# Kernel optimization log

Hardware: AMD Instinct MI355X
Metric: run time of the kernel (lower is better)

Reference implementation:

```python
import jax, jax.numpy as jnp
import numpy as np
from jax import lax

EPS = 1e-4
DN = ('NDHWC', 'DHWIO', 'NDHWC')


def _m(mask, dtype):
    return mask[..., None].astype(dtype)


def bn_relu(x, mask):
    # BatchNorm1d over active voxels only (training-mode batch stats, gamma=1, beta=0), then ReLU.
    m = _m(mask, x.dtype)
    n = jnp.sum(m)
    mean = jnp.sum(x * m, axis=(0, 1, 2, 3)) / n
    xc = (x - mean) * m  # re-mask: inactive voxels stay exactly zero
    var = jnp.sum(xc * xc, axis=(0, 1, 2, 3)) / n
    return jnp.maximum(xc * lax.rsqrt(var + EPS), 0.0)


def subm3(x, w, mask):
    # SubMConv3d k=3 pad=1: dense conv on zero-at-inactive input, output restricted to active sites.
    y = lax.conv_general_dilated(x, w, (1, 1, 1), 'SAME', dimension_numbers=DN)
    return y * _m(mask, x.dtype)


def down2(x, w):
    # SparseConv3d k=2 s=2: non-overlapping windows; inactive inputs are zero so dense strided conv matches.
    return lax.conv_general_dilated(x, w, (2, 2, 2), 'VALID', dimension_numbers=DN)


def pool_mask(mask):
    B, D, H, W = mask.shape
    return jnp.any(mask.reshape(B, D // 2, 2, H // 2, 2, W // 2, 2), axis=(2, 4, 6))


def up2(x, w, mask):
    # SparseInverseConv3d k=2 (indice_key inverse of the stride-2 conv): conv-transpose masked to original indices.
    y = jnp.einsum('bdhwc,ijkco->bdihjwko', x, w)
    B, Dc, _, Hc, _, Wc, _, Co = y.shape
    return y.reshape(B, 2 * Dc, 2 * Hc, 2 * Wc, Co) * _m(mask, x.dtype)


def resblock(x, mask, wa, wb, w_sc=None):
    # ResidualBlock: i_branch (identity or 1x1 Custom1x1Subm3d: feats @ W.T) + BN-ReLU-SubM-BN-ReLU-SubM.
    idb = x if w_sc is None else jnp.einsum('bdhwc,oc->bdhwo', x, w_sc)
    h = bn_relu(x, mask)
    h = subm3(h, wa, mask)
    h = bn_relu(h, mask)
    h = subm3(h, wb, mask)
    return h + idb


def unet_forward(x, mask, w_in, w_b1a, w_b1b, w_d1, w_b2a, w_b2b, w_d2,
                 w_b3a, w_b3b, w_u2, w_t2_sc, w_t2a, w_t2b, w_u1, w_t1_sc, w_t1a, w_t1b):
    mask2 = pool_mask(mask)
    mask3 = pool_mask(mask2)
    x0 = subm3(x, w_in, mask)                 # input_conv (subm1)
    x1 = resblock(x0, mask, w_b1a, w_b1b)     # level-1 block (32->32)
    d1 = down2(bn_relu(x1, mask), w_d1)       # BN-ReLU + stride-2 conv 32->64
    x2 = resblock(d1, mask2, w_b2a, w_b2b)    # level-2 block (64->64)
    d2 = down2(bn_relu(x2, mask2), w_d2)      # 64->96
    x3 = resblock(d2, mask3, w_b3a, w_b3b)    # bottom level (96->96)
    u2 = up2(bn_relu(x3, mask3), w_u2, mask2)  # BN-ReLU + inverse conv 96->64
    t2 = resblock(jnp.concatenate([x2, u2], -1), mask2, w_t2a, w_t2b, w_t2_sc)  # tail 128->64
    u1 = up2(bn_relu(t2, mask2), w_u1, mask)   # 64->32
    t1 = resblock(jnp.concatenate([x1, u1], -1), mask, w_t1a, w_t1b, w_t1_sc)   # tail 64->32
    return bn_relu(t1, mask)                   # output_layer: BN + ReLU


def setup_inputs() -> dict:
    key = jax.random.key(0)
    ks = jax.random.split(key, 20)
    B, D = 1, 48
    Cin, C1, C2, C3 = 6, 32, 64, 96
    mask = jax.random.uniform(ks[0], (B, D, D, D)) < 0.12
    x = jax.random.normal(ks[1], (B, D, D, D, Cin), jnp.float32) * mask[..., None]

    def w(k, shape):
        fan = float(np.prod(shape[:-1]))
        return (jax.random.normal(k, shape, jnp.float32) / np.sqrt(fan)).astype(jnp.float32)

    return {
        'x': x, 'mask': mask,
        'w_in': w(ks[2], (3, 3, 3, Cin, C1)),
        'w_b1a': w(ks[3], (3, 3, 3, C1, C1)), 'w_b1b': w(ks[4], (3, 3, 3, C1, C1)),
        'w_d1': w(ks[5], (2, 2, 2, C1, C2)),
        'w_b2a': w(ks[6], (3, 3, 3, C2, C2)), 'w_b2b': w(ks[7], (3, 3, 3, C2, C2)),
        'w_d2': w(ks[8], (2, 2, 2, C2, C3)),
        'w_b3a': w(ks[9], (3, 3, 3, C3, C3)), 'w_b3b': w(ks[10], (3, 3, 3, C3, C3)),
        'w_u2': w(ks[11], (2, 2, 2, C3, C2)),
        'w_t2_sc': w(ks[12], (C2, 2 * C2)),
        'w_t2a': w(ks[13], (3, 3, 3, 2 * C2, C2)), 'w_t2b': w(ks[14], (3, 3, 3, C2, C2)),
        'w_u1': w(ks[15], (2, 2, 2, C2, C1)),
        'w_t1_sc': w(ks[16], (C1, 2 * C1)),
        'w_t1a': w(ks[17], (3, 3, 3, 2 * C1, C1)), 'w_t1b': w(ks[18], (3, 3, 3, C1, C1)),
    }


def reference(x, mask, w_in, w_b1a, w_b1b, w_d1, w_b2a, w_b2b, w_d2,
              w_b3a, w_b3b, w_u2, w_t2_sc, w_t2a, w_t2b, w_u1, w_t1_sc, w_t1a, w_t1b):
    return unet_forward(x, mask, w_in, w_b1a, w_b1b, w_d1, w_b2a, w_b2b, w_d2,
                        w_b3a, w_b3b, w_u2, w_t2_sc, w_t2a, w_t2b, w_u1, w_t1_sc, w_t1a, w_t1b)
```

## Files before the change

kernel.cpp:

```cpp
#include <hip/hip_runtime.h>


typedef short bf16x8 __attribute__((ext_vector_type(8)));
typedef float f32x4 __attribute__((ext_vector_type(4)));
typedef unsigned short ushort_t;

constexpr int D1 = 48, DIM2 = 24, DIM3 = 12;
constexpr int N1 = D1 * D1 * D1;
constexpr int N2 = DIM2 * DIM2 * DIM2;
constexpr int N3 = DIM3 * DIM3 * DIM3;

constexpr size_t OFF_A      = 0;
constexpr size_t OFF_R1     = 3538944;
constexpr size_t OFF_CAT1   = 7077888;
constexpr size_t OFF_D1R    = 14155776;
constexpr size_t OFF_R3     = 15040512;
constexpr size_t OFF_CAT2   = 15925248;
constexpr size_t OFF_D2R    = 17694720;
constexpr size_t OFF_R4     = 17860608;
constexpr size_t OFF_X3R    = 18026496;
constexpr size_t OFF_BN1_32 = 18192384;
constexpr size_t OFF_BN1_64 = 19961920;
constexpr size_t OFF_BN2_64 = 23500928;
constexpr size_t OFF_BN2_128= 23943360;
constexpr size_t OFF_BN3_96 = 24828160;
constexpr size_t OFF_BFEND  = 24911168;
constexpr size_t OFF_WT     = 24911168;
constexpr size_t OFF_STATS  = 25634112;
constexpr size_t STATS_FLOATS = 15 * 2048 * 2;
constexpr size_t OFF_CNT    = OFF_STATS + STATS_FLOATS;
constexpr size_t OFF_L1     = OFF_CNT + 16;
constexpr size_t OFF_L2     = OFF_L1 + N1;
constexpr size_t OFF_L3     = OFF_L2 + N2;
constexpr size_t OFF_M1     = OFF_L3 + N3;
constexpr size_t OFF_M2     = OFF_M1 + N1 / 4;
constexpr size_t OFF_M3     = OFF_M2 + N2 / 4;

constexpr int WTS[16] = {0, 32768, 65536, 98304, 114688, 229376, 344064,
                         393216, 669696, 946176, 1175552, 1290240, 1347584,
                         1380352, 1429504, 1445888};

__device__ inline ushort_t f2bf(float f) {
  union { float f; unsigned u; } x; x.f = f;
  unsigned u = x.u + 0x7FFF + ((x.u >> 16) & 1);
  return (ushort_t)(u >> 16);
}

__global__ __launch_bounds__(256) void k_mask1(const float* __restrict__ x,
                                               unsigned char* __restrict__ m,
                                               int* __restrict__ list, int* __restrict__ cnt) {
  int v = blockIdx.x * 256 + threadIdx.x;
  if (v >= N1) return;
  const float* p = x + (size_t)v * 6;
  bool a = (p[0] != 0.f) || (p[1] != 0.f) || (p[2] != 0.f) ||
           (p[3] != 0.f) || (p[4] != 0.f) || (p[5] != 0.f);
  m[v] = a ? 1 : 0;
  if (a) { int pos = atomicAdd(cnt, 1); list[pos] = v; }
}

__global__ __launch_bounds__(256) void k_pool(const unsigned char* __restrict__ mf,
                                              unsigned char* __restrict__ mc,
                                              int* __restrict__ list, int* __restrict__ cnt, int DC) {
  int v = blockIdx.x * 256 + threadIdx.x;
  int n = DC * DC * DC;
  if (v >= n) return;
  int w = v % DC, h = (v / DC) % DC, d = v / (DC * DC);
  int DF = 2 * DC;
  bool a = false;
  for (int i = 0; i < 2; i++)
    for (int j = 0; j < 2; j++)
      for (int k = 0; k < 2; k++)
        a |= (mf[(size_t)(((2 * d + i) * DF + (2 * h + j)) * DF + (2 * w + k))] != 0);
  mc[v] = a ? 1 : 0;
  if (a) { int pos = atomicAdd(cnt, 1); list[pos] = v; }
}

struct WJobs {
  const float* src[15];
  int start[16];
  short cinr[15], cipad[15], cout[15], kk[15];
};

__global__ __launch_bounds__(256) void k_wprep(WJobs jb, ushort_t* __restrict__ wt, int total) {
  int gid = blockIdx.x * 256 + threadIdx.x;
  if (gid >= total) return;
  int j = 0;
#pragma unroll
  for (int jj = 0; jj < 15; jj++)
    if (gid >= jb.start[jj + 1]) j = jj + 1;
  int e = gid - jb.start[j];
  int CIP = jb.cipad[j], CO = jb.cout[j], CIR = jb.cinr[j], KKr = jb.kk[j];
  int ci = e % CIP;
  int co = (e / CIP) % CO;
  int k = e / (CIP * CO);
  float v = (k < KKr && ci < CIR) ? jb.src[j][((size_t)k * CIR + ci) * CO + co] : 0.f;
  wt[gid] = f2bf(v);
}

__global__ __launch_bounds__(256) void k_xprep(const float* __restrict__ x, ushort_t* __restrict__ xp) {
  int gid = blockIdx.x * 256 + threadIdx.x;
  if (gid >= (N1 + 4) * 8) return;
  int v = gid >> 3, c = (gid & 7) * 4;
  uint2 o = make_uint2(0u, 0u);
  if (v < N1) {
    ushort_t u[4];
#pragma unroll
    for (int j = 0; j < 4; j++) {
      int ci = c + j;
      float f = (ci < 6) ? x[(size_t)v * 6 + ci] : 0.f;
      u[j] = f2bf(f);
    }
    o.x = (unsigned)u[0] | ((unsigned)u[1] << 16);
    o.y = (unsigned)u[2] | ((unsigned)u[3] << 16);
  }
  *(uint2*)&xp[(size_t)v * 32 + c] = o;
}

template <int CIPAD, int COUT, int KK, bool UP>
__global__ __launch_bounds__(512, 2) void k_conv6(
    const ushort_t* __restrict__ in, const ushort_t* __restrict__ wt,
    float* __restrict__ out, int ostride, int ooff,
    const float* __restrict__ res, int rstride,
    double* __restrict__ st,
    const int* __restrict__ list, const int* __restrict__ cnt, int DD) {
  constexpr int KCH = CIPAD / 32;
  constexpr int TPS = (KK + 3) / 4;
  __shared__ float red[8][8][64];
  __shared__ float fin[32][33];
  __shared__ int vidx[32];

  int n = cnt[0];
  int base = blockIdx.x * 32;
  if (base >= n) return;
  int t = threadIdx.x, wv = t >> 6, ln = t & 63;
  int vg = wv & 1, ks = wv >> 1;
  int fr = ln & 15, kg = ln >> 4;
  int coblk = blockIdx.y * 32;
  if (t < 32) vidx[t] = (base + t < n) ? list[base + t] : -1;

  int ai = base + vg * 16 + fr;
  int av = (ai < n) ? list[ai] : -1;
  int vv = av < 0 ? 0 : av;
  int ad = vv / (DD * DD), ah = (vv / DD) % DD, aw = vv % DD;
  int pidx = 0, corner = 0;
  if (UP) {
    int DC = DD / 2;
    pidx = (((ad >> 1) * DC) + (ah >> 1)) * DC + (aw >> 1);
    corner = ((ad & 1) << 2) | ((ah & 1) << 1) | (aw & 1);
  }
  const int GDI = UP ? (DD >> 1) : ((KK == 8) ? 2 * DD : DD);
  const int SENT = GDI * GDI * GDI;

  int k0 = ks * TPS;

  auto nixOf = [&](int k) -> int {
    int kc = (k < KK) ? k : KK - 1;
    if (UP) {
      return (av >= 0 && corner == kc) ? pidx : SENT;
    } else if (KK == 27) {
      int kd = kc / 9 - 1, kh = (kc / 3) % 3 - 1, kw = kc % 3 - 1;
      int nd = ad + kd, nh = ah + kh, nw = aw + kw;
      bool inb = (av >= 0) && (unsigned)nd < (unsigned)DD &&
                 (unsigned)nh < (unsigned)DD && (unsigned)nw < (unsigned)DD;
      return inb ? (nd * DD + nh) * DD + nw : SENT;
    } else {
      return (av >= 0) ? ((2 * ad + ((kc >> 2) & 1)) * GDI + (2 * ah + ((kc >> 1) & 1))) * GDI +
                             (2 * aw + (kc & 1))
                       : SENT;
    }
  };

  f32x4 acc0 = (f32x4){0.f, 0.f, 0.f, 0.f};
  f32x4 acc1 = (f32x4){0.f, 0.f, 0.f, 0.f};

  bf16x8 aX[KCH], bX[2 * KCH], aY[KCH], bY[2 * KCH];

#define LOADSET(AR, BR, J)                                                         \
  {                                                                                \
    int kk_ = k0 + (J);                                                            \
    int nix_ = nixOf(kk_);                                                         \
    const ushort_t* ap_ = in + (size_t)nix_ * CIPAD + kg * 8;                      \
    _Pragma("unroll") for (int c = 0; c < KCH; c++)                                \
        AR[c] = *(const bf16x8*)(ap_ + c * 32);                                    \
    const ushort_t* wb_ = wt + ((size_t)(kk_ * COUT + coblk + fr)) * CIPAD + kg * 8; \
    _Pragma("unroll") for (int c = 0; c < KCH; c++) {                              \
      BR[c] = *(const bf16x8*)(wb_ + c * 32);                                      \
      BR[KCH + c] = *(const bf16x8*)(wb_ + (size_t)16 * CIPAD + c * 32);           \
    }                                                                              \
  }
#define MFMASET(AR, BR)                                                            \
  _Pragma("unroll") for (int c = 0; c < KCH; c++) {                                \
    acc0 = __builtin_amdgcn_mfma_f32_16x16x32_bf16(AR[c], BR[c], acc0, 0, 0, 0);   \
    acc1 = __builtin_amdgcn_mfma_f32_16x16x32_bf16(AR[c], BR[KCH + c], acc1, 0, 0, 0); \
  }

  LOADSET(aX, bX, 0);
#pragma unroll
  for (int j = 0; j < TPS; j += 2) {
    if (j + 1 < TPS) LOADSET(aY, bY, j + 1);
    MFMASET(aX, bX);
    if (j + 2 < TPS) LOADSET(aX, bX, j + 2);
    if (j + 1 < TPS) MFMASET(aY, bY);
  }
#undef LOADSET
#undef MFMASET

#pragma unroll
  for (int r = 0; r < 4; r++) {
    red[wv][r][ln] = acc0[r];
    red[wv][4 + r][ln] = acc1[r];
  }
  __syncthreads();
#pragma unroll
  for (int e0 = 0; e0 < 2; e0++) {
    int e = t + e0 * 512;
    int ln2 = e & 63, r = (e >> 6) & 3, f = (e >> 8) & 1, vg2 = e >> 9;
    int ei = f * 4 + r;
    float s = red[vg2][ei][ln2] + red[2 + vg2][ei][ln2] +
              red[4 + vg2][ei][ln2] + red[6 + vg2][ei][ln2];
    int fr2 = ln2 & 15, kg2 = ln2 >> 4;
    int slot = vg2 * 16 + kg2 * 4 + r;
    int co = f * 16 + fr2;
    int v = vidx[slot];
    float val = 0.f;
    if (v >= 0) {
      int gco = coblk + co;
      val = s;
      if (res) val += res[(size_t)v * rstride + gco];
      out[(size_t)v * ostride + ooff + gco] = val;
    }
    fin[slot][co] = val;
  }
  __syncthreads();
  if (t < 32) {
    float sm = 0.f, sq = 0.f;
#pragma unroll
    for (int p = 0; p < 32; p++) {
      float x = fin[p][t];
      sm += x; sq += x * x;
    }
    double* sr = st + (size_t)(blockIdx.x & 7) * 256;
    atomicAdd(&sr[coblk + t], (double)sm);
    atomicAdd(&sr[128 + coblk + t], (double)sq);
  }
}

template <int C>
__global__ __launch_bounds__(256) void k_bnapply2(
    const float* __restrict__ x, int xstr,
    const double* __restrict__ sA, const double* __restrict__ sB, int csplit,
    const int* __restrict__ list, const int* __restrict__ cnt,
    ushort_t* __restrict__ out) {
  __shared__ float mu_s[C], inv_s[C];
  int n = cnt[0];
  int t = threadIdx.x;
  if (t < C) {
    const double* s = (t < csplit) ? (sA + t) : (sB + (t - csplit));
    double sm = 0.0, sq = 0.0;
#pragma unroll
    for (int r = 0; r < 8; r++) { sm += s[r * 256]; sq += s[r * 256 + 128]; }
    double mu = sm / n;
    double var = sq / n - mu * mu;
    mu_s[t] = (float)mu;
    inv_s[t] = rsqrtf((float)fmax(var, 0.0) + 1e-4f);
  }
  __syncthreads();
  int total = n * (C / 4);
  for (int gid = blockIdx.x * 256 + t; gid < total; gid += gridDim.x * 256) {
    int i = gid / (C / 4);
    int c = (gid % (C / 4)) * 4;
    int v = list[i];
    float4 xv = *(const float4*)&x[(size_t)v * xstr + c];
    float xa[4] = {xv.x, xv.y, xv.z, xv.w};
    ushort_t u[4];
#pragma unroll
    for (int j = 0; j < 4; j++)
      u[j] = f2bf(fmaxf((xa[j] - mu_s[c + j]) * inv_s[c + j], 0.f));
    uint2 o; o.x = (unsigned)u[0] | ((unsigned)u[1] << 16);
    o.y = (unsigned)u[2] | ((unsigned)u[3] << 16);
    *(uint2*)&out[(size_t)v * C + c] = o;
  }
}

__global__ __launch_bounds__(256) void k_bnout(const float* __restrict__ x,
                                               const unsigned char* __restrict__ m,
                                               const double* __restrict__ s,
                                               const int* __restrict__ cnt,
                                               float* __restrict__ out) {
  __shared__ float mu_s[32], inv_s[32];
  int t = threadIdx.x;
  int n = cnt[0];
  if (t < 32) {
    double sm = 0.0, sq = 0.0;
#pragma unroll
    for (int r = 0; r < 8; r++) { sm += s[r * 256 + t]; sq += s[r * 256 + 128 + t]; }
    double mu = sm / n;
    double var = sq / n - mu * mu;
    mu_s[t] = (float)mu;
    inv_s[t] = rsqrtf((float)fmax(var, 0.0) + 1e-4f);
  }
  __syncthreads();
  int gid = blockIdx.x * 256 + t;
  if (gid >= N1 * 8) return;
  int v = gid / 8;
  int c = (gid % 8) * 4;
  float4 o = make_float4(0.f, 0.f, 0.f, 0.f);
  if (m[v]) {
    float4 xv = *(const float4*)&x[(size_t)v * 32 + c];
    o.x = fmaxf((xv.x - mu_s[c + 0]) * inv_s[c + 0], 0.f);
    o.y = fmaxf((xv.y - mu_s[c + 1]) * inv_s[c + 1], 0.f);
    o.z = fmaxf((xv.z - mu_s[c + 2]) * inv_s[c + 2], 0.f);
    o.w = fmaxf((xv.w - mu_s[c + 3]) * inv_s[c + 3], 0.f);
  }
  *(float4*)&out[(size_t)v * 32 + c] = o;
}

template <int CI, int CO>
__global__ __launch_bounds__(256) void k_sc(const float* __restrict__ in,
                                            const float* __restrict__ wsc,
                                            float* __restrict__ out,
                                            const int* __restrict__ list,
                                            const int* __restrict__ cnt) {
  int n = cnt[0];
  long total = (long)n * CO;
  for (long gid = (long)blockIdx.x * 256 + threadIdx.x; gid < total; gid += (long)gridDim.x * 256) {
    int i = (int)(gid / CO), o = (int)(gid % CO);
    int v = list[i];
    const float4* xr = (const float4*)(in + (size_t)v * CI);
    const float4* wr = (const float4*)(wsc + (size_t)o * CI);
    float a = 0.f;
    for (int c = 0; c < CI / 4; c++) {
      float4 x4 = xr[c], w4 = wr[c];
      a += x4.x * w4.x + x4.y * w4.y + x4.z * w4.z + x4.w * w4.w;
    }
    out[(size_t)v * CO + o] = a;
  }
}

extern "C" void kernel_launch(void* const* d_in, const int* in_sizes, int n_in,
                              void* d_out, int out_size, void* d_ws, size_t ws_size,
                              hipStream_t stream) {
  float* W = (float*)d_ws;
  const float* x = (const float*)d_in[0];

  float* A    = W + OFF_A;
  float* R1   = W + OFF_R1;
  float* CAT1 = W + OFF_CAT1;
  float* D1R  = W + OFF_D1R;
  float* R3   = W + OFF_R3;
  float* CAT2 = W + OFF_CAT2;
  float* D2R  = W + OFF_D2R;
  float* R4   = W + OFF_R4;
  float* X3R  = W + OFF_X3R;
  ushort_t* XP     = (ushort_t*)(W + OFF_CAT1);
  ushort_t* BN1_32 = (ushort_t*)(W + OFF_BN1_32);
  ushort_t* BN1_64 = (ushort_t*)(W + OFF_BN1_64);
  ushort_t* BN2_64 = (ushort_t*)(W + OFF_BN2_64);
  ushort_t* BN2_128= (ushort_t*)(W + OFF_BN2_128);
  ushort_t* BN3_96 = (ushort_t*)(W + OFF_BN3_96);
  ushort_t* WT  = (ushort_t*)(W + OFF_WT);
  double* S0 = (double*)(W + OFF_STATS);
  int* CNT = (int*)(W + OFF_CNT);
  int* L1 = (int*)(W + OFF_L1);
  int* L2 = (int*)(W + OFF_L2);
  int* L3 = (int*)(W + OFF_L3);
  unsigned char* M1 = (unsigned char*)(W + OFF_M1);
  unsigned char* M2 = (unsigned char*)(W + OFF_M2);
  unsigned char* M3 = (unsigned char*)(W + OFF_M3);

  auto S = [&](int i) { return S0 + (size_t)i * 2048; };

  hipMemsetAsync(W + OFF_STATS, 0, (STATS_FLOATS + 16) * 4, stream);
  hipMemsetAsync(W + OFF_BN1_32, 0, (OFF_BFEND - OFF_BN1_32) * 4, stream);

  k_mask1<<<N1 / 256, 256, 0, stream>>>(x, M1, L1, CNT + 0);
  k_pool<<<N2 / 256, 256, 0, stream>>>(M1, M2, L2, CNT + 1, DIM2);
  k_pool<<<(N3 + 255) / 256, 256, 0, stream>>>(M2, M3, L3, CNT + 2, DIM3);

  WJobs jb;
  const int srcIdx[15] = {2, 3, 4, 5, 6, 7, 8, 9, 10, 13, 14, 17, 18, 11, 15};
  const short cinr[15]  = {6, 32, 32, 32, 64, 64, 64, 96, 96, 128, 64, 64, 32, 96, 64};
  const short cipad[15] = {32, 32, 32, 32, 64, 64, 64, 96, 96, 128, 64, 64, 32, 96, 64};
  const short couts[15] = {32, 32, 32, 64, 64, 64, 96, 96, 96, 64, 64, 32, 32, 64, 32};
  const short kkr[15]   = {27, 27, 27, 8, 27, 27, 8, 27, 27, 27, 27, 27, 27, 8, 8};
  for (int j = 0; j < 15; j++) {
    jb.src[j] = (const float*)d_in[srcIdx[j]];
    jb.cinr[j] = cinr[j]; jb.cipad[j] = cipad[j]; jb.cout[j] = couts[j];
    jb.kk[j] = kkr[j];
    jb.start[j] = WTS[j];
  }
  jb.start[15] = WTS[15];
  k_wprep<<<(WTS[15] + 255) / 256, 256, 0, stream>>>(jb, WT, WTS[15]);
  k_xprep<<<((N1 + 4) * 8 + 255) / 256, 256, 0, stream>>>(x, XP);

  const int GB1 = 512, GB2 = 320, GB3 = 54;
  const int BNG = 512;

  k_conv6<32, 32, 27, false><<<dim3(GB1, 1), 512, 0, stream>>>(
      XP, WT + WTS[0], A, 32, 0, nullptr, 0, S(0), L1, CNT + 0, D1);
  k_bnapply2<32><<<BNG, 256, 0, stream>>>(A, 32, S(0), S(0), 32, L1, CNT + 0, BN1_32);
  k_conv6<32, 32, 27, false><<<dim3(GB1, 1), 512, 0, stream>>>(
      BN1_32, WT + WTS[1], R1, 32, 0, nullptr, 0, S(1), L1, CNT + 0, D1);
  k_bnapply2<32><<<BNG, 256, 0, stream>>>(R1, 32, S(1), S(1), 32, L1, CNT + 0, BN1_32);
  k_conv6<32, 32, 27, false><<<dim3(GB1, 1), 512, 0, stream>>>(
      BN1_32, WT + WTS[2], CAT1, 64, 0, A, 32, S(2), L1, CNT + 0, D1);
  k_bnapply2<32><<<BNG, 256, 0, stream>>>(CAT1, 64, S(2), S(2), 32, L1, CNT + 0, BN1_32);
  k_conv6<32, 64, 8, false><<<dim3(GB2, 2), 512, 0, stream>>>(
      BN1_32, WT + WTS[3], D1R, 64, 0, nullptr, 0, S(3), L2, CNT + 1, DIM2);

  k_bnapply2<64><<<BNG, 256, 0, stream>>>(D1R, 64, S(3), S(3), 64, L2, CNT + 1, BN2_64);
  k_conv6<64, 64, 27, false><<<dim3(GB2, 2), 512, 0, stream>>>(
      BN2_64, WT + WTS[4], R3, 64, 0, nullptr, 0, S(4), L2, CNT + 1, DIM2);
  k_bnapply2<64><<<BNG, 256, 0, stream>>>(R3, 64, S(4), S(4), 64, L2, CNT + 1, BN2_64);
  k_conv6<64, 64, 27, false><<<dim3(GB2, 2), 512, 0, stream>>>(
      BN2_64, WT + WTS[5], CAT2, 128, 0, D1R, 64, S(5), L2, CNT + 1, DIM2);
  k_bnapply2<64><<<BNG, 256, 0, stream>>>(CAT2, 128, S(5), S(5), 64, L2, CNT + 1, BN2_64);
  k_conv6<64, 96, 8, false><<<dim3(GB3, 3), 512, 0, stream>>>(
      BN2_64, WT + WTS[6], D2R, 96, 0, nullptr, 0, S(6), L3, CNT + 2, DIM3);

  k_bnapply2<96><<<BNG, 256, 0, stream>>>(D2R, 96, S(6), S(6), 96, L3, CNT + 2, BN3_96);
  k_conv6<96, 96, 27, false><<<dim3(GB3, 3), 512, 0, stream>>>(
      BN3_96, WT + WTS[7], R4, 96, 0, nullptr, 0, S(7), L3, CNT + 2, DIM3);
  k_bnapply2<96><<<BNG, 256, 0, stream>>>(R4, 96, S(7), S(7), 96, L3, CNT + 2, BN3_96);
  k_conv6<96, 96, 27, false><<<dim3(GB3, 3), 512, 0, stream>>>(
      BN3_96, WT + WTS[8], X3R, 96, 0, D2R, 96, S(8), L3, CNT + 2, DIM3);
  k_bnapply2<96><<<BNG, 256, 0, stream>>>(X3R, 96, S(8), S(8), 96, L3, CNT + 2, BN3_96);
  k_conv6<96, 64, 8, true><<<dim3(GB2, 2), 512, 0, stream>>>(
      BN3_96, WT + WTS[13], CAT2, 128, 64, nullptr, 0, S(9), L2, CNT + 1, DIM2);

  k_bnapply2<128><<<BNG, 256, 0, stream>>>(CAT2, 128, S(5), S(9), 64, L2, CNT + 1, BN2_128);
  k_conv6<128, 64, 27, false><<<dim3(GB2, 2), 512, 0, stream>>>(
      BN2_128, WT + WTS[9], R3, 64, 0, nullptr, 0, S(10), L2, CNT + 1, DIM2);
  k_bnapply2<64><<<BNG, 256, 0, stream>>>(R3, 64, S(10), S(10), 64, L2, CNT + 1, BN2_64);
  k_sc<128, 64><<<512, 256, 0, stream>>>(CAT2, (const float*)d_in[12], D1R, L2, CNT + 1);
  k_conv6<64, 64, 27, false><<<dim3(GB2, 2), 512, 0, stream>>>(
      BN2_64, WT + WTS[10], R3, 64, 0, D1R, 64, S(11), L2, CNT + 1, DIM2);
  k_bnapply2<64><<<BNG, 256, 0, stream>>>(R3, 64, S(11), S(11), 64, L2, CNT + 1, BN2_64);
  k_conv6<64, 32, 8, true><<<dim3(GB1, 1), 512, 0, stream>>>(
      BN2_64, WT + WTS[14], CAT1, 64, 32, nullptr, 0, S(12), L1, CNT + 0, D1);

  k_bnapply2<64><<<BNG, 256, 0, stream>>>(CAT1, 64, S(2), S(12), 32, L1, CNT + 0, BN1_64);
  k_conv6<64, 32, 27, false><<<dim3(GB1, 1), 512, 0, stream>>>(
      BN1_64, WT + WTS[11], R1, 32, 0, nullptr, 0, S(13), L1, CNT + 0, D1);
  k_bnapply2<32><<<BNG, 256, 0, stream>>>(R1, 32, S(13), S(13), 32, L1, CNT + 0, BN1_32);
  k_sc<64, 32><<<512, 256, 0, stream>>>(CAT1, (const float*)d_in[16], A, L1, CNT + 0);
  k_conv6<32, 32, 27, false><<<dim3(GB1, 1), 512, 0, stream>>>(
      BN1_32, WT + WTS[12], A, 32, 0, A, 32, S(14), L1, CNT + 0, D1);
  k_bnout<<<N1 * 8 / 256, 256, 0, stream>>>(A, M1, S(14), CNT + 0, (float*)d_out);
}
```

Baseline: 418.8 us.

## Stage conv weights in LDS and loop persistent blocks over voxel tiles

Replaces the conv kernel with a version that copies each block's full weight slice (all taps, a CB-wide output-channel chunk) into shared memory once, then loops persistently over 32-voxel tiles, reading B operands from LDS instead of global memory. BN statistics are now accumulated per thread across tiles and reduced through shared atomics, replacing the per-tile 32x33 final reduction. The 128-channel decoder conv is split into two 64-channel convs (the second accumulating onto the first through the residual input), so smaller LDS weight tiles and BN buffers can be used. The cost is a large LDS footprint per block that may limit occupancy, plus an extra launch and an extra read/write of R3 for the split conv.

```diff
diff --git a/kernel.cpp b/kernel.cpp
--- a/kernel.cpp
+++ b/kernel.cpp
@@ -21,13 +21,13 @@
 constexpr size_t OFF_X3R    = 18026496;
 constexpr size_t OFF_BN1_32 = 18192384;
 constexpr size_t OFF_BN1_64 = 19961920;
-constexpr size_t OFF_BN2_64 = 23500928;
-constexpr size_t OFF_BN2_128= 23943360;
-constexpr size_t OFF_BN3_96 = 24828160;
-constexpr size_t OFF_BFEND  = 24911168;
-constexpr size_t OFF_WT     = 24911168;
-constexpr size_t OFF_STATS  = 25634112;
-constexpr size_t STATS_FLOATS = 15 * 2048 * 2;
+constexpr size_t OFF_BN2_A  = 23500928;
+constexpr size_t OFF_BN2_B  = 23943360;
+constexpr size_t OFF_BN3_96 = 24385792;
+constexpr size_t OFF_BFEND  = 24468800;
+constexpr size_t OFF_WT     = 24468800;
+constexpr size_t OFF_STATS  = 25142592;
+constexpr size_t STATS_FLOATS = 16 * 4096;
 constexpr size_t OFF_CNT    = OFF_STATS + STATS_FLOATS;
 constexpr size_t OFF_L1     = OFF_CNT + 16;
 constexpr size_t OFF_L2     = OFF_L1 + N1;
@@ -36,9 +36,9 @@
 constexpr size_t OFF_M2     = OFF_M1 + N1 / 4;
 constexpr size_t OFF_M3     = OFF_M2 + N2 / 4;
 
-constexpr int WTS[16] = {0, 32768, 65536, 98304, 114688, 229376, 344064,
-                         393216, 669696, 946176, 1175552, 1290240, 1347584,
-                         1380352, 1429504, 1445888};
+constexpr int WTS[17] = {0, 27648, 55296, 82944, 99328, 209920, 320512,
+                         369664, 618496, 867328, 977920, 1088512, 1199104,
+                         1254400, 1282048, 1331200, 1347584};
 
 __device__ inline ushort_t f2bf(float f) {
   union { float f; unsigned u; } x; x.f = f;
@@ -76,9 +76,9 @@
 }
 
 struct WJobs {
-  const float* src[15];
-  int start[16];
-  short cinr[15], cipad[15], cout[15], kk[15];
+  const float* src[16];
+  int start[17];
+  short cirtot[16], cio[16], cipad[16], cout[16];
 };
 
 __global__ __launch_bounds__(256) void k_wprep(WJobs jb, ushort_t* __restrict__ wt, int total) {
@@ -86,14 +86,15 @@
   if (gid >= total) return;
   int j = 0;
 #pragma unroll
-  for (int jj = 0; jj < 15; jj++)
+  for (int jj = 0; jj < 16; jj++)
     if (gid >= jb.start[jj + 1]) j = jj + 1;
   int e = gid - jb.start[j];
-  int CIP = jb.cipad[j], CO = jb.cout[j], CIR = jb.cinr[j], KKr = jb.kk[j];
+  int CIP = jb.cipad[j], CO = jb.cout[j];
+  int CIRT = jb.cirtot[j], CIO = jb.cio[j];
   int ci = e % CIP;
   int co = (e / CIP) % CO;
   int k = e / (CIP * CO);
-  float v = (k < KKr && ci < CIR) ? jb.src[j][((size_t)k * CIR + ci) * CO + co] : 0.f;
+  float v = (ci + CIO < CIRT) ? jb.src[j][((size_t)k * CIRT + CIO + ci) * CO + co] : 0.f;
   wt[gid] = f2bf(v);
 }
 
@@ -116,138 +117,151 @@
   *(uint2*)&xp[(size_t)v * 32 + c] = o;
 }
 
-template <int CIPAD, int COUT, int KK, bool UP>
-__global__ __launch_bounds__(512, 2) void k_conv6(
-    const ushort_t* __restrict__ in, const ushort_t* __restrict__ wt,
+template <int CIPAD, int CB, int KK, int DD, bool UP>
+__global__ __launch_bounds__(512, 2) void k_conv7(
+    const ushort_t* __restrict__ in, const ushort_t* __restrict__ wt, int cot,
     float* __restrict__ out, int ostride, int ooff,
     const float* __restrict__ res, int rstride,
     double* __restrict__ st,
-    const int* __restrict__ list, const int* __restrict__ cnt, int DD) {
+    const int* __restrict__ list, const int* __restrict__ cnt) {
   constexpr int KCH = CIPAD / 32;
+  constexpr int NCO = CB / 16;
   constexpr int TPS = (KK + 3) / 4;
-  __shared__ float red[8][8][64];
-  __shared__ float fin[32][33];
+  constexpr int BUNITS = KK * KCH * CB * 4;
+  __shared__ ushort_t blds[BUNITS * 8];
+  __shared__ float red[4][2][NCO * 4][64];
+  __shared__ float sred0[CB], sred1[CB];
   __shared__ int vidx[32];
 
   int n = cnt[0];
-  int base = blockIdx.x * 32;
-  if (base >= n) return;
   int t = threadIdx.x, wv = t >> 6, ln = t & 63;
   int vg = wv & 1, ks = wv >> 1;
   int fr = ln & 15, kg = ln >> 4;
-  int coblk = blockIdx.y * 32;
-  if (t < 32) vidx[t] = (base + t < n) ? list[base + t] : -1;
-
-  int ai = base + vg * 16 + fr;
-  int av = (ai < n) ? list[ai] : -1;
-  int vv = av < 0 ? 0 : av;
-  int ad = vv / (DD * DD), ah = (vv / DD) % DD, aw = vv % DD;
-  int pidx = 0, corner = 0;
-  if (UP) {
-    int DC = DD / 2;
-    pidx = (((ad >> 1) * DC) + (ah >> 1)) * DC + (aw >> 1);
-    corner = ((ad & 1) << 2) | ((ah & 1) << 1) | (aw & 1);
-  }
-  const int GDI = UP ? (DD >> 1) : ((KK == 8) ? 2 * DD : DD);
-  const int SENT = GDI * GDI * GDI;
-
-  int k0 = ks * TPS;
-
-  auto nixOf = [&](int k) -> int {
-    int kc = (k < KK) ? k : KK - 1;
+  int coblk = blockIdx.y * CB;
+
+  for (int e = t; e < BUNITS; e += 512) {
+    int kgs = e & 3;
+    int co = (e >> 2) % CB;
+    int r2 = (e >> 2) / CB;
+    int c = r2 % KCH;
+    int k = r2 / KCH;
+    bf16x8 w = *(const bf16x8*)(wt + ((size_t)k * cot + coblk + co) * CIPAD + c * 32 + kgs * 8);
+    *(bf16x8*)(blds + (size_t)e * 8) = w;
+  }
+  if (t < CB) { sred0[t] = 0.f; sred1[t] = 0.f; }
+  __syncthreads();
+
+  float smr = 0.f, sqr = 0.f;
+  int myco = ((t >> 8) % NCO) * 16 + (t & 15);
+
+  for (int tile = blockIdx.x; tile * 32 < n; tile += gridDim.x) {
+    int base = tile * 32;
+    if (t < 32) vidx[t] = (base + t < n) ? list[base + t] : -1;
+    __syncthreads();
+
+    int av = vidx[vg * 16 + fr];
+    int vv = av < 0 ? 0 : av;
+    int ad = vv / (DD * DD), ah = (vv / DD) % DD, aw = vv % DD;
+    int pidx = 0, corner = -1;
     if (UP) {
-      return (av >= 0 && corner == kc) ? pidx : SENT;
-    } else if (KK == 27) {
-      int kd = kc / 9 - 1, kh = (kc / 3) % 3 - 1, kw = kc % 3 - 1;
-      int nd = ad + kd, nh = ah + kh, nw = aw + kw;
-      bool inb = (av >= 0) && (unsigned)nd < (unsigned)DD &&
-                 (unsigned)nh < (unsigned)DD && (unsigned)nw < (unsigned)DD;
-      return inb ? (nd * DD + nh) * DD + nw : SENT;
-    } else {
-      return (av >= 0) ? ((2 * ad + ((kc >> 2) & 1)) * GDI + (2 * ah + ((kc >> 1) & 1))) * GDI +
-                             (2 * aw + (kc & 1))
-                       : SENT;
+      constexpr int DC = DD / 2;
+      pidx = (((ad >> 1) * DC) + (ah >> 1)) * DC + (aw >> 1);
+      corner = ((ad & 1) << 2) | ((ah & 1) << 1) | (aw & 1);
     }
-  };
-
-  f32x4 acc0 = (f32x4){0.f, 0.f, 0.f, 0.f};
-  f32x4 acc1 = (f32x4){0.f, 0.f, 0.f, 0.f};
-
-  bf16x8 aX[KCH], bX[2 * KCH], aY[KCH], bY[2 * KCH];
-
-#define LOADSET(AR, BR, J)                                                         \
-  {                                                                                \
-    int kk_ = k0 + (J);                                                            \
-    int nix_ = nixOf(kk_);                                                         \
-    const ushort_t* ap_ = in + (size_t)nix_ * CIPAD + kg * 8;                      \
-    _Pragma("unroll") for (int c = 0; c < KCH; c++)                                \
-        AR[c] = *(const bf16x8*)(ap_ + c * 32);                                    \
-    const ushort_t* wb_ = wt + ((size_t)(kk_ * COUT + coblk + fr)) * CIPAD + kg * 8; \
-    _Pragma("unroll") for (int c = 0; c < KCH; c++) {                              \
-      BR[c] = *(const bf16x8*)(wb_ + c * 32);                                      \
-      BR[KCH + c] = *(const bf16x8*)(wb_ + (size_t)16 * CIPAD + c * 32);           \
-    }                                                                              \
-  }
-#define MFMASET(AR, BR)                                                            \
-  _Pragma("unroll") for (int c = 0; c < KCH; c++) {                                \
-    acc0 = __builtin_amdgcn_mfma_f32_16x16x32_bf16(AR[c], BR[c], acc0, 0, 0, 0);   \
-    acc1 = __builtin_amdgcn_mfma_f32_16x16x32_bf16(AR[c], BR[KCH + c], acc1, 0, 0, 0); \
-  }
-
-  LOADSET(aX, bX, 0);
-#pragma unroll
-  for (int j = 0; j < TPS; j += 2) {
-    if (j + 1 < TPS) LOADSET(aY, bY, j + 1);
-    MFMASET(aX, bX);
-    if (j + 2 < TPS) LOADSET(aX, bX, j + 2);
-    if (j + 1 < TPS) MFMASET(aY, bY);
-  }
-#undef LOADSET
-#undef MFMASET
-
-#pragma unroll
-  for (int r = 0; r < 4; r++) {
-    red[wv][r][ln] = acc0[r];
-    red[wv][4 + r][ln] = acc1[r];
-  }
+    constexpr int GDI = UP ? (DD / 2) : ((KK == 8) ? 2 * DD : DD);
+    constexpr int SENT = GDI * GDI * GDI;
+
+    const int k0 = ks * TPS;
+    auto nixOf = [&](int kq) -> int {
+      int kc = (kq < KK) ? kq : KK - 1;
+      if (UP) {
+        return (av >= 0 && corner == kc) ? pidx : SENT;
+      } else if (KK == 27) {
+        int kd = kc / 9 - 1, kh = (kc / 3) % 3 - 1, kw = kc % 3 - 1;
+        int nd = ad + kd, nh = ah + kh, nw = aw + kw;
+        bool inb = (av >= 0) && (unsigned)nd < (unsigned)DD &&
+                   (unsigned)nh < (unsigned)DD && (unsigned)nw < (unsigned)DD;
+        return inb ? (nd * DD + nh) * DD + nw : SENT;
+      } else {
+        return (av >= 0) ? ((2 * ad + ((kc >> 2) & 1)) * GDI + (2 * ah + ((kc >> 1) & 1))) * GDI +
+                               (2 * aw + (kc & 1))
+                         : SENT;
+      }
+    };
+    auto loadA = [&](bf16x8* dst, int kq) {
+      int nix = nixOf(kq);
+      const ushort_t* ap = in + (size_t)nix * CIPAD + kg * 8;
+#pragma unroll
+      for (int c = 0; c < KCH; c++) dst[c] = *(const bf16x8*)(ap + c * 32);
+    };
+
+    f32x4 acc[NCO];
+#pragma unroll
+    for (int f = 0; f < NCO; f++) acc[f] = (f32x4){0.f, 0.f, 0.f, 0.f};
+
+    bf16x8 aA[KCH], aB[KCH];
+    loadA(aA, k0);
+#pragma unroll
+    for (int j = 0; j < TPS; j++) {
+      bf16x8* cur = (j & 1) ? aB : aA;
+      bf16x8* nxt = (j & 1) ? aA : aB;
+      if (j + 1 < TPS) loadA(nxt, k0 + j + 1);
+      if (k0 + j < KK) {
+#pragma unroll
+        for (int c = 0; c < KCH; c++) {
+#pragma unroll
+          for (int f = 0; f < NCO; f++) {
+            bf16x8 b = *(const bf16x8*)(blds +
+                ((((size_t)((k0 + j) * KCH + c) * CB) + f * 16 + fr) * 4 + kg) * 8);
+            acc[f] = __builtin_amdgcn_mfma_f32_16x16x32_bf16(cur[c], b, acc[f], 0, 0, 0);
+          }
+        }
+      }
+    }
+
+#pragma unroll
+    for (int f = 0; f < NCO; f++)
+#pragma unroll
+      for (int r = 0; r < 4; r++)
+        red[ks][vg][f * 4 + r][ln] = acc[f][r];
+    __syncthreads();
+
+#pragma unroll
+    for (int e0 = 0; e0 < NCO; e0++) {
+      int e = t + e0 * 512;
+      int ln2 = e & 63, r = (e >> 6) & 3;
+      int f = (e >> 8) % NCO;
+      int vg2 = e / (256 * NCO);
+      int ei = f * 4 + r;
+      float s = red[0][vg2][ei][ln2] + red[1][vg2][ei][ln2] +
+                red[2][vg2][ei][ln2] + red[3][vg2][ei][ln2];
+      int slot = vg2 * 16 + (ln2 >> 4) * 4 + r;
+      int co = f * 16 + (ln2 & 15);
+      int v = vidx[slot];
+      if (v >= 0) {
+        int gco = coblk + co;
+        float val = s;
+        if (res) val += res[(size_t)v * rstride + gco];
+        out[(size_t)v * ostride + ooff + gco] = val;
+        smr += val; sqr += val * val;
+      }
+    }
+    __syncthreads();
+  }
+
+  atomicAdd(&sred0[myco], smr);
+  atomicAdd(&sred1[myco], sqr);
   __syncthreads();
-#pragma unroll
-  for (int e0 = 0; e0 < 2; e0++) {
-    int e = t + e0 * 512;
-    int ln2 = e & 63, r = (e >> 6) & 3, f = (e >> 8) & 1, vg2 = e >> 9;
-    int ei = f * 4 + r;
-    float s = red[vg2][ei][ln2] + red[2 + vg2][ei][ln2] +
-              red[4 + vg2][ei][ln2] + red[6 + vg2][ei][ln2];
-    int fr2 = ln2 & 15, kg2 = ln2 >> 4;
-    int slot = vg2 * 16 + kg2 * 4 + r;
-    int co = f * 16 + fr2;
-    int v = vidx[slot];
-    float val = 0.f;
-    if (v >= 0) {
-      int gco = coblk + co;
-      val = s;
-      if (res) val += res[(size_t)v * rstride + gco];
-      out[(size_t)v * ostride + ooff + gco] = val;
-    }
-    fin[slot][co] = val;
-  }
-  __syncthreads();
-  if (t < 32) {
-    float sm = 0.f, sq = 0.f;
-#pragma unroll
-    for (int p = 0; p < 32; p++) {
-      float x = fin[p][t];
-      sm += x; sq += x * x;
-    }
+  if (t < CB) {
     double* sr = st + (size_t)(blockIdx.x & 7) * 256;
-    atomicAdd(&sr[coblk + t], (double)sm);
-    atomicAdd(&sr[128 + coblk + t], (double)sq);
+    atomicAdd(&sr[coblk + t], (double)sred0[t]);
+    atomicAdd(&sr[128 + coblk + t], (double)sred1[t]);
   }
 }
 
 template <int C>
 __global__ __launch_bounds__(256) void k_bnapply2(
-    const float* __restrict__ x, int xstr,
+    const float* __restrict__ x, int xstr, int coff,
     const double* __restrict__ sA, const double* __restrict__ sB, int csplit,
     const int* __restrict__ list, const int* __restrict__ cnt,
     ushort_t* __restrict__ out) {
@@ -270,7 +284,7 @@
     int i = gid / (C / 4);
     int c = (gid % (C / 4)) * 4;
     int v = list[i];
-    float4 xv = *(const float4*)&x[(size_t)v * xstr + c];
+    float4 xv = *(const float4*)&x[(size_t)v * xstr + coff + c];
     float xa[4] = {xv.x, xv.y, xv.z, xv.w};
     ushort_t u[4];
 #pragma unroll
@@ -355,8 +369,8 @@
   ushort_t* XP     = (ushort_t*)(W + OFF_CAT1);
   ushort_t* BN1_32 = (ushort_t*)(W + OFF_BN1_32);
   ushort_t* BN1_64 = (ushort_t*)(W + OFF_BN1_64);
-  ushort_t* BN2_64 = (ushort_t*)(W + OFF_BN2_64);
-  ushort_t* BN2_128= (ushort_t*)(W + OFF_BN2_128);
+  ushort_t* BN2A   = (ushort_t*)(W + OFF_BN2_A);
+  ushort_t* BN2B   = (ushort_t*)(W + OFF_BN2_B);
   ushort_t* BN3_96 = (ushort_t*)(W + OFF_BN3_96);
   ushort_t* WT  = (ushort_t*)(W + OFF_WT);
   double* S0 = (double*)(W + OFF_STATS);
@@ -378,73 +392,74 @@
   k_pool<<<(N3 + 255) / 256, 256, 0, stream>>>(M2, M3, L3, CNT + 2, DIM3);
 
   WJobs jb;
-  const int srcIdx[15] = {2, 3, 4, 5, 6, 7, 8, 9, 10, 13, 14, 17, 18, 11, 15};
-  const short cinr[15]  = {6, 32, 32, 32, 64, 64, 64, 96, 96, 128, 64, 64, 32, 96, 64};
-  const short cipad[15] = {32, 32, 32, 32, 64, 64, 64, 96, 96, 128, 64, 64, 32, 96, 64};
-  const short couts[15] = {32, 32, 32, 64, 64, 64, 96, 96, 96, 64, 64, 32, 32, 64, 32};
-  const short kkr[15]   = {27, 27, 27, 8, 27, 27, 8, 27, 27, 27, 27, 27, 27, 8, 8};
-  for (int j = 0; j < 15; j++) {
+  const int srcIdx[16]  = {2, 3, 4, 5, 6, 7, 8, 9, 10, 13, 13, 14, 17, 18, 11, 15};
+  const short cirtot[16]= {6, 32, 32, 32, 64, 64, 64, 96, 96, 128, 128, 64, 64, 32, 96, 64};
+  const short cio[16]   = {0, 0, 0, 0, 0, 0, 0, 0, 0, 0, 64, 0, 0, 0, 0, 0};
+  const short cipad[16] = {32, 32, 32, 32, 64, 64, 64, 96, 96, 64, 64, 64, 64, 32, 96, 64};
+  const short couts[16] = {32, 32, 32, 64, 64, 64, 96, 96, 96, 64, 64, 64, 32, 32, 64, 32};
+  for (int j = 0; j < 16; j++) {
     jb.src[j] = (const float*)d_in[srcIdx[j]];
-    jb.cinr[j] = cinr[j]; jb.cipad[j] = cipad[j]; jb.cout[j] = couts[j];
-    jb.kk[j] = kkr[j];
+    jb.cirtot[j] = cirtot[j]; jb.cio[j] = cio[j];
+    jb.cipad[j] = cipad[j]; jb.cout[j] = couts[j];
     jb.start[j] = WTS[j];
   }
-  jb.start[15] = WTS[15];
-  k_wprep<<<(WTS[15] + 255) / 256, 256, 0, stream>>>(jb, WT, WTS[15]);
+  jb.start[16] = WTS[16];
+  k_wprep<<<(WTS[16] + 255) / 256, 256, 0, stream>>>(jb, WT, WTS[16]);
   k_xprep<<<((N1 + 4) * 8 + 255) / 256, 256, 0, stream>>>(x, XP);
 
-  const int GB1 = 512, GB2 = 320, GB3 = 54;
   const int BNG = 512;
 
-  k_conv6<32, 32, 27, false><<<dim3(GB1, 1), 512, 0, stream>>>(
-      XP, WT + WTS[0], A, 32, 0, nullptr, 0, S(0), L1, CNT + 0, D1);
-  k_bnapply2<32><<<BNG, 256, 0, stream>>>(A, 32, S(0), S(0), 32, L1, CNT + 0, BN1_32);
-  k_conv6<32, 32, 27, false><<<dim3(GB1, 1), 512, 0, stream>>>(
-      BN1_32, WT + WTS[1], R1, 32, 0, nullptr, 0, S(1), L1, CNT + 0, D1);
-  k_bnapply2<32><<<BNG, 256, 0, stream>>>(R1, 32, S(1), S(1), 32, L1, CNT + 0, BN1_32);
-  k_conv6<32, 32, 27, false><<<dim3(GB1, 1), 512, 0, stream>>>(
-      BN1_32, WT + WTS[2], CAT1, 64, 0, A, 32, S(2), L1, CNT + 0, D1);
-  k_bnapply2<32><<<BNG, 256, 0, stream>>>(CAT1, 64, S(2), S(2), 32, L1, CNT + 0, BN1_32);
-  k_conv6<32, 64, 8, false><<<dim3(GB2, 2), 512, 0, stream>>>(
-      BN1_32, WT + WTS[3], D1R, 64, 0, nullptr, 0, S(3), L2, CNT + 1, DIM2);
-
-  k_bnapply2<64><<<BNG, 256, 0, stream>>>(D1R, 64, S(3), S(3), 64, L2, CNT + 1, BN2_64);
-  k_conv6<64, 64, 27, false><<<dim3(GB2, 2), 512, 0, stream>>>(
-      BN2_64, WT + WTS[4], R3, 64, 0, nullptr, 0, S(4), L2, CNT + 1, DIM2);
-  k_bnapply2<64><<<BNG, 256, 0, stream>>>(R3, 64, S(4), S(4), 64, L2, CNT + 1, BN2_64);
-  k_conv6<64, 64, 27, false><<<dim3(GB2, 2), 512, 0, stream>>>(
-      BN2_64, WT + WTS[5], CAT2, 128, 0, D1R, 64, S(5), L2, CNT + 1, DIM2);
-  k_bnapply2<64><<<BNG, 256, 0, stream>>>(CAT2, 128, S(5), S(5), 64, L2, CNT + 1, BN2_64);
-  k_conv6<64, 96, 8, false><<<dim3(GB3, 3), 512, 0, stream>>>(
-      BN2_64, WT + WTS[6], D2R, 96, 0, nullptr, 0, S(6), L3, CNT + 2, DIM3);
-
-  k_bnapply2<96><<<BNG, 256, 0, stream>>>(D2R, 96, S(6), S(6), 96, L3, CNT + 2, BN3_96);
-  k_conv6<96, 96, 27, false><<<dim3(GB3, 3), 512, 0, stream>>>(
-      BN3_96, WT + WTS[7], R4, 96, 0, nullptr, 0, S(7), L3, CNT + 2, DIM3);
-  k_bnapply2<96><<<BNG, 256, 0, stream>>>(R4, 96, S(7), S(7), 96, L3, CNT + 2, BN3_96);
-  k_conv6<96, 96, 27, false><<<dim3(GB3, 3), 512, 0, stream>>>(
-      BN3_96, WT + WTS[8], X3R, 96, 0, D2R, 96, S(8), L3, CNT + 2, DIM3);
-  k_bnapply2<96><<<BNG, 256, 0, stream>>>(X3R, 96, S(8), S(8), 96, L3, CNT + 2, BN3_96);
-  k_conv6<96, 64, 8, true><<<dim3(GB2, 2), 512, 0, stream>>>(
-      BN3_96, WT + WTS[13], CAT2, 128, 64, nullptr, 0, S(9), L2, CNT + 1, DIM2);
-
-  k_bnapply2<128><<<BNG, 256, 0, stream>>>(CAT2, 128, S(5), S(9), 64, L2, CNT + 1, BN2_128);
-  k_conv6<128, 64, 27, false><<<dim3(GB2, 2), 512, 0, stream>>>(
-      BN2_128, WT + WTS[9], R3, 64, 0, nullptr, 0, S(10), L2, CNT + 1, DIM2);
-  k_bnapply2<64><<<BNG, 256, 0, stream>>>(R3, 64, S(10), S(10), 64, L2, CNT + 1, BN2_64);
+  k_conv7<32, 32, 27, D1, false><<<dim3(256, 1), 512, 0, stream>>>(
+      XP, WT + WTS[0], 32, A, 32, 0, nullptr, 0, S(0), L1, CNT + 0);
+  k_bnapply2<32><<<BNG, 256, 0, stream>>>(A, 32, 0, S(0), S(0), 32, L1, CNT + 0, BN1_32);
+  k_conv7<32, 32, 27, D1, false><<<dim3(256, 1), 512, 0, stream>>>(
+      BN1_32, WT + WTS[1], 32, R1, 32, 0, nullptr, 0, S(1), L1, CNT + 0);
+  k_bnapply2<32><<<BNG, 256, 0, stream>>>(R1, 32, 0, S(1), S(1), 32, L1, CNT + 0, BN1_32);
+  k_conv7<32, 32, 27, D1, false><<<dim3(256, 1), 512, 0, stream>>>(
+      BN1_32, WT + WTS[2], 32, CAT1, 64, 0, A, 32, S(2), L1, CNT + 0);
+  k_bnapply2<32><<<BNG, 256, 0, stream>>>(CAT1, 64, 0, S(2), S(2), 32, L1, CNT + 0, BN1_32);
+  k_conv7<32, 32, 8, DIM2, false><<<dim3(128, 2), 512, 0, stream>>>(
+      BN1_32, WT + WTS[3], 64, D1R, 64, 0, nullptr, 0, S(3), L2, CNT + 1);
+
+  k_bnapply2<64><<<BNG, 256, 0, stream>>>(D1R, 64, 0, S(3), S(3), 64, L2, CNT + 1, BN2A);
+  k_conv7<64, 32, 27, DIM2, false><<<dim3(128, 2), 512, 0, stream>>>(
+      BN2A, WT + WTS[4], 64, R3, 64, 0, nullptr, 0, S(4), L2, CNT + 1);
+  k_bnapply2<64><<<BNG, 256, 0, stream>>>(R3, 64, 0, S(4), S(4), 64, L2, CNT + 1, BN2A);
+  k_conv7<64, 32, 27, DIM2, false><<<dim3(128, 2), 512, 0, stream>>>(
+      BN2A, WT + WTS[5], 64, CAT2, 128, 0, D1R, 64, S(5), L2, CNT + 1);
+  k_bnapply2<64><<<BNG, 256, 0, stream>>>(CAT2, 128, 0, S(5), S(5), 64, L2, CNT + 1, BN2A);
+  k_conv7<64, 32, 8, DIM3, false><<<dim3(54, 3), 512, 0, stream>>>(
+      BN2A, WT + WTS[6], 96, D2R, 96, 0, nullptr, 0, S(6), L3, CNT + 2);
+
+  k_bnapply2<96><<<BNG, 256, 0, stream>>>(D2R, 96, 0, S(6), S(6), 96, L3, CNT + 2, BN3_96);
+  k_conv7<96, 16, 27, DIM3, false><<<dim3(54, 6), 512, 0, stream>>>(
+      BN3_96, WT + WTS[7], 96, R4, 96, 0, nullptr, 0, S(7), L3, CNT + 2);
+  k_bnapply2<96><<<BNG, 256, 0, stream>>>(R4, 96, 0, S(7), S(7), 96, L3, CNT + 2, BN3_96);
+  k_conv7<96, 16, 27, DIM3, false><<<dim3(54, 6), 512, 0, stream>>>(
+      BN3_96, WT + WTS[8], 96, X3R, 96, 0, D2R, 96, S(8), L3, CNT + 2);
+  k_bnapply2<96><<<BNG, 256, 0, stream>>>(X3R, 96, 0, S(8), S(8), 96, L3, CNT + 2, BN3_96);
+  k_conv7<96, 32, 8, DIM2, true><<<dim3(128, 2), 512, 0, stream>>>(
+      BN3_96, WT + WTS[14], 64, CAT2, 128, 64, nullptr, 0, S(9), L2, CNT + 1);
+
+  k_bnapply2<64><<<BNG, 256, 0, stream>>>(CAT2, 128, 64, S(9), S(9), 64, L2, CNT + 1, BN2B);
+  k_conv7<64, 32, 27, DIM2, false><<<dim3(128, 2), 512, 0, stream>>>(
+      BN2A, WT + WTS[9], 64, R3, 64, 0, nullptr, 0, S(15), L2, CNT + 1);
+  k_conv7<64, 32, 27, DIM2, false><<<dim3(128, 2), 512, 0, stream>>>(
+      BN2B, WT + WTS[10], 64, R3, 64, 0, R3, 64, S(10), L2, CNT + 1);
+  k_bnapply2<64><<<BNG, 256, 0, stream>>>(R3, 64, 0, S(10), S(10), 64, L2, CNT + 1, BN2A);
   k_sc<128, 64><<<512, 256, 0, stream>>>(CAT2, (const float*)d_in[12], D1R, L2, CNT + 1);
-  k_conv6<64, 64, 27, false><<<dim3(GB2, 2), 512, 0, stream>>>(
-      BN2_64, WT + WTS[10], R3, 64, 0, D1R, 64, S(11), L2, CNT + 1, DIM2);
-  k_bnapply2<64><<<BNG, 256, 0, stream>>>(R3, 64, S(11), S(11), 64, L2, CNT + 1, BN2_64);
-  k_conv6<64, 32, 8, true><<<dim3(GB1, 1), 512, 0, stream>>>(
-      BN2_64, WT + WTS[14], CAT1, 64, 32, nullptr, 0, S(12), L1, CNT + 0, D1);
-
-  k_bnapply2<64><<<BNG, 256, 0, stream>>>(CAT1, 64, S(2), S(12), 32, L1, CNT + 0, BN1_64);
-  k_conv6<64, 32, 27, false><<<dim3(GB1, 1), 512, 0, stream>>>(
-      BN1_64, WT + WTS[11], R1, 32, 0, nullptr, 0, S(13), L1, CNT + 0, D1);
-  k_bnapply2<32><<<BNG, 256, 0, stream>>>(R1, 32, S(13), S(13), 32, L1, CNT + 0, BN1_32);
+  k_conv7<64, 32, 27, DIM2, false><<<dim3(128, 2), 512, 0, stream>>>(
+      BN2A, WT + WTS[11], 64, R3, 64, 0, D1R, 64, S(11), L2, CNT + 1);
+  k_bnapply2<64><<<BNG, 256, 0, stream>>>(R3, 64, 0, S(11), S(11), 64, L2, CNT + 1, BN2A);
+  k_conv7<64, 32, 8, D1, true><<<dim3(256, 1), 512, 0, stream>>>(
+      BN2A, WT + WTS[15], 32, CAT1, 64, 32, nullptr, 0, S(12), L1, CNT + 0);
+
+  k_bnapply2<64><<<BNG, 256, 0, stream>>>(CAT1, 64, 0, S(2), S(12), 32, L1, CNT + 0, BN1_64);
+  k_conv7<64, 32, 27, D1, false><<<dim3(256, 1), 512, 0, stream>>>(
+      BN1_64, WT + WTS[12], 32, R1, 32, 0, nullptr, 0, S(13), L1, CNT + 0);
+  k_bnapply2<32><<<BNG, 256, 0, stream>>>(R1, 32, 0, S(13), S(13), 32, L1, CNT + 0, BN1_32);
   k_sc<64, 32><<<512, 256, 0, stream>>>(CAT1, (const float*)d_in[16], A, L1, CNT + 0);
-  k_conv6<32, 32, 27, false><<<dim3(GB1, 1), 512, 0, stream>>>(
-      BN1_32, WT + WTS[12], A, 32, 0, A, 32, S(14), L1, CNT + 0, D1);
+  k_conv7<32, 32, 27, D1, false><<<dim3(256, 1), 512, 0, stream>>>(
+      BN1_32, WT + WTS[13], 32, A, 32, 0, A, 32, S(14), L1, CNT + 0);
   k_bnout<<<N1 * 8 / 256, 256, 0, stream>>>(A, M1, S(14), CNT + 0, (float*)d_out);
 }
```

Measured after the change: 391.6 us. 6.5% less time.
